# Performance work log

Measured on AMD Instinct MI355X. Metric: run time of the kernel, lower is better.

## Reference

```python
import jax, jax.numpy as jnp
import numpy as np

C = 1024
T = 2048
B = 8

def setup_inputs() -> dict:
    key = jax.random.key(0)
    ks = jax.random.split(key, 7)
    s = lambda fan_in: 1.0 / np.sqrt(fan_in)
    return {
        "x":     jax.random.normal(ks[0], (B, T, C), dtype=jnp.float32),
        "w_qkv": jax.random.uniform(ks[1], (C, 3 * C), jnp.float32, -s(C), s(C)),
        "w_proj": jax.random.uniform(ks[2], (C, C), jnp.float32, -s(C), s(C)),
        "w1":    jax.random.uniform(ks[3], (C, 2 * C), jnp.float32, -s(C), s(C)),
        "w2":    jax.random.uniform(ks[4], (2 * C, C), jnp.float32, -s(2 * C), s(2 * C)),
        "g1":    jnp.ones((C,), jnp.float32),
        "g2":    jnp.ones((C,), jnp.float32),
    }

def rmsnorm(x, g, eps=1e-6):
    return x * jax.lax.rsqrt(jnp.mean(x * x, axis=-1, keepdims=True) + eps) * g

def reference(x, w_qkv, w_proj, w1, w2, g1, g2):
    t = x.shape[1]
    # --- attention ---
    h = rmsnorm(x, g1)
    qkv = h @ w_qkv                               # [B,T,3C]
    q, k, v = jnp.split(qkv, 3, axis=-1)
    scores = jnp.einsum('bqc,bkc->bqk', q, k) * (C ** -0.5)  # [B,T,T]
    causal = jnp.triu(jnp.ones((t, t), dtype=bool), k=1)
    scores = jnp.where(causal, -jnp.inf, scores)
    attn = jax.nn.softmax(scores, axis=-1)
    x = x + (attn @ v) @ w_proj
    # --- ffn ---
    h = rmsnorm(x, g2)
    return x + (jax.nn.silu(h @ w1)) @ w2
```

## Files before the change

kernel.cpp:

```cpp
#include <hip/hip_runtime.h>
#include <hip/hip_bf16.h>
#include <stdint.h>


#define C_DIM 1024
#define T_DIM 2048
#define B_DIM 8

typedef float f32x4  __attribute__((ext_vector_type(4)));
typedef float f32x16 __attribute__((ext_vector_type(16)));
typedef __bf16 bf16x8 __attribute__((ext_vector_type(8)));

typedef const __attribute__((address_space(1))) void gvoid_t;
typedef __attribute__((address_space(3))) void lvoid_t;

__device__ __forceinline__ void gload_lds16(const void* g, void* l) {
    __builtin_amdgcn_global_load_lds((gvoid_t*)g, (lvoid_t*)l, 16, 0, 0);
}

__device__ __forceinline__ unsigned short f2bf_bits(float f) {
    __hip_bfloat16 h = __float2bfloat16(f);
    return *reinterpret_cast<unsigned short*>(&h);
}

__device__ __forceinline__ void xcd_remap(int& bx, int& by, int& bz) {
    const int gx = gridDim.x, gy = gridDim.y;
    const int nwg = gx * gy * (int)gridDim.z;
    const int orig = bx + gx * (by + gy * bz);
    const int q = nwg >> 3, r = nwg & 7;
    const int xcd = orig & 7, pos = orig >> 3;
    const int neu = (xcd < r ? xcd * (q + 1) : r * (q + 1) + (xcd - r) * q) + pos;
    bx = neu % gx;
    const int t = neu / gx;
    by = t % gy;
    bz = t / gy;
}

#define RD_A(dst, buf, hq) do { \
    _Pragma("unroll") \
    for (int mf_ = 0; mf_ < 4; ++mf_) { \
        const char* p_ = lds + (buf)*32768 + wrb + (hq)*8192 + mf_*2048; \
        dst[mf_][0] = *(const bf16x8*)(p_ + offk0); \
        dst[mf_][1] = *(const bf16x8*)(p_ + offk1); \
    } \
} while(0)

#define RD_B(dst, buf, nh) do { \
    _Pragma("unroll") \
    for (int n2_ = 0; n2_ < 2; ++n2_) { \
        const char* p_ = lds + 65536 + (buf)*32768 + wcb + ((nh)*2 + n2_)*2048; \
        dst[n2_][0] = *(const bf16x8*)(p_ + offk0); \
        dst[n2_][1] = *(const bf16x8*)(p_ + offk1); \
    } \
} while(0)

#define MMQ(aS, bS, Mh, Nh) do { \
    _Pragma("unroll") \
    for (int m4_ = 0; m4_ < 4; ++m4_) \
    _Pragma("unroll") \
    for (int n2_ = 0; n2_ < 2; ++n2_) \
    _Pragma("unroll") \
    for (int ks_ = 0; ks_ < 2; ++ks_) \
        acc[(Mh)*4 + m4_][(Nh)*2 + n2_] = __builtin_amdgcn_mfma_f32_16x16x32_bf16( \
            aS[m4_][ks_], bS[n2_][ks_], acc[(Mh)*4 + m4_][(Nh)*2 + n2_], 0, 0, 0); \
} while(0)

#define STA(buf, half, kt) do { \
    const int go_ = aoff + (half)*128*lda + (kt)*64; \
    char* lp_ = ldsw + (buf)*32768 + (half)*16384; \
    gload_lds16(A + go_,            lp_); \
    gload_lds16(A + go_ + 64*lda,   lp_ + 8192); \
} while(0)
#define STB(buf, half, kt) do { \
    const int go_ = boff + (half)*128*ldb + (kt)*64; \
    char* lp_ = ldsw + 65536 + (buf)*32768 + (half)*16384; \
    gload_lds16(Bt + go_,           lp_); \
    gload_lds16(Bt + go_ + 64*ldb,  lp_ + 8192); \
} while(0)

#define TILE_BODY(t, STG) do { \
    const int buf_ = (t) & 1; \
    bf16x8 a0[4][2], a1[4][2], b0v[2][2], b1v[2][2]; \
    RD_A(a0, buf_, 0); RD_A(a1, buf_, 1); \
    RD_B(b0v, buf_, 0); RD_B(b1v, buf_, 1); \
    __builtin_amdgcn_s_setprio(1); \
    MMQ(a0, b0v, 0, 0); MMQ(a0, b1v, 0, 1); \
    MMQ(a1, b0v, 1, 0); MMQ(a1, b1v, 1, 1); \
    __builtin_amdgcn_s_setprio(0); \
    asm volatile("s_waitcnt lgkmcnt(0)" ::: "memory"); \
    asm volatile("s_waitcnt vmcnt(0)" ::: "memory"); \
    __builtin_amdgcn_s_barrier(); \
    if (STG) { STB(buf_,0,(t)+2); STB(buf_,1,(t)+2); \
               STA(buf_,0,(t)+2); STA(buf_,1,(t)+2); } \
} while(0)

template<int EPI>
__global__ __launch_bounds__(512, 2)
void gemm256(const __hip_bfloat16* A, const __hip_bfloat16* Bt,
             void* Cout, const void* Rv,
             int K, int lda, int ldb, int ldc)
{
    int bx = blockIdx.x, by = blockIdx.y, bz = blockIdx.z;
    xcd_remap(bx, by, bz);

    const int tid  = threadIdx.x;
    const int lane = tid & 63, wave = tid >> 6;
    const int l15  = lane & 15, l4 = lane >> 4;
    const int wr   = wave >> 2, wc = wave & 3;
    const int m0   = by * 256, n0 = bx * 256;

    __shared__ __align__(16) char lds_[131072];
    char* lds  = lds_;
    char* ldsw = lds_ + wave * 1024;

    const int NT = K >> 6;

    const int offk0 = l15 * 128 + (((l4)     ^ (l15 & 7)) << 4);
    const int offk1 = l15 * 128 + (((4 + l4) ^ (l15 & 7)) << 4);
    const int wrb = wr * 16384, wcb = wc * 8192;

    const int rowq  = tid >> 3;
    const int sslot = (tid & 7) ^ (rowq & 7);
    const int aoff  = (m0 + rowq) * lda + sslot * 8;
    const int boff  = (n0 + rowq) * ldb + sslot * 8;

    f32x4 acc[8][4];
#pragma unroll
    for (int i = 0; i < 8; ++i)
#pragma unroll
        for (int j = 0; j < 4; ++j) acc[i][j] = (f32x4){0.f, 0.f, 0.f, 0.f};

    STB(0, 0, 0); STB(0, 1, 0); STA(0, 0, 0); STA(0, 1, 0);
    STB(1, 0, 1); STB(1, 1, 1); STA(1, 0, 1); STA(1, 1, 1);
    asm volatile("s_waitcnt vmcnt(8)" ::: "memory");
    __builtin_amdgcn_s_barrier();

    int t = 0;
    for (; t < NT - 2; ++t) TILE_BODY(t, true);
    for (; t < NT; ++t)     TILE_BODY(t, false);

    asm volatile("s_waitcnt vmcnt(0)" ::: "memory");

#pragma unroll
    for (int mf = 0; mf < 8; ++mf) {
        const int rbase = m0 + wr * 128 + mf * 16 + l4 * 4;
#pragma unroll
        for (int nf = 0; nf < 4; ++nf) {
            const int col = n0 + wc * 64 + nf * 16 + l15;
#pragma unroll
            for (int r = 0; r < 4; ++r) {
                const float v = acc[mf][nf][r];
                const int row = rbase + r;
                if constexpr (EPI == 5) {
                    ((__hip_bfloat16*)Cout)[((long long)(row >> 11) * C_DIM + col) * T_DIM
                                            + (row & 2047)] = __float2bfloat16(v);
                } else {
                    const long long idx = (long long)row * ldc + col;
                    if constexpr (EPI == 0) {
                        ((__hip_bfloat16*)Cout)[idx] = __float2bfloat16(v);
                    } else if constexpr (EPI == 3) {
                        const float s = v / (1.f + __expf(-v));
                        ((__hip_bfloat16*)Cout)[idx] = __float2bfloat16(s);
                    } else if constexpr (EPI == 8) {
                        const float xr = ((const float*)Rv)[idx];
                        ((__hip_bfloat16*)Cout)[idx] = __float2bfloat16(v + xr);
                    } else {
                        const float xr =
                            __bfloat162float(((const __hip_bfloat16*)Rv)[idx]);
                        ((float*)Cout)[idx] = v + xr;
                    }
                }
            }
        }
    }
}

__global__ __launch_bounds__(512, 2)
void gemm256_w32(const __hip_bfloat16* A, const __hip_bfloat16* Bt,
                 void* Cout, int K, int lda, int ldb, int ldc)
{
    int bx = blockIdx.x, by = blockIdx.y, bz = blockIdx.z;
    xcd_remap(bx, by, bz);

    const int tid  = threadIdx.x;
    const int lane = tid & 63, wave = tid >> 6;
    const int l31  = lane & 31, l5 = lane >> 5;
    const int wr   = wave >> 2, wc = wave & 3;
    const int m0   = by * 256, n0 = bx * 256;

    __shared__ __align__(16) char lds_[131072];
    char* lds  = lds_;
    char* ldsw = lds_ + wave * 1024;

    const int NT = K >> 6;

    const int rowq  = tid >> 3;
    const int sslot = (tid & 7) ^ (rowq & 7);
    const int aoff  = (m0 + rowq) * lda + sslot * 8;
    const int boff  = (n0 + rowq) * ldb + sslot * 8;

    f32x16 acc[4][2];
#pragma unroll
    for (int i = 0; i < 4; ++i)
#pragma unroll
        for (int j = 0; j < 2; ++j)
#pragma unroll
            for (int e = 0; e < 16; ++e) acc[i][j][e] = 0.f;

    const int arowl = l31 & 7;

    STB(0, 0, 0); STB(0, 1, 0); STA(0, 0, 0); STA(0, 1, 0);
    STB(1, 0, 1); STB(1, 1, 1); STA(1, 0, 1); STA(1, 1, 1);
    asm volatile("s_waitcnt vmcnt(8)" ::: "memory");
    __builtin_amdgcn_s_barrier();

    for (int t = 0; t < NT; ++t) {
        const int buf_ = t & 1;
        bf16x8 aR[4][4], bR[2][4];
#pragma unroll
        for (int mf = 0; mf < 4; ++mf) {
            const int arow = wr * 128 + mf * 32 + l31;
            const char* p_ = lds + buf_ * 32768 + arow * 128;
#pragma unroll
            for (int ks = 0; ks < 4; ++ks)
                aR[mf][ks] = *(const bf16x8*)(p_ + ((((ks << 1) | l5) ^ arowl) << 4));
        }
#pragma unroll
        for (int nf = 0; nf < 2; ++nf) {
            const int bcol = wc * 64 + nf * 32 + l31;
            const char* p_ = lds + 65536 + buf_ * 32768 + bcol * 128;
#pragma unroll
            for (int ks = 0; ks < 4; ++ks)
                bR[nf][ks] = *(const bf16x8*)(p_ + ((((ks << 1) | l5) ^ arowl) << 4));
        }
        __builtin_amdgcn_s_setprio(1);
#pragma unroll
        for (int mf = 0; mf < 4; ++mf)
#pragma unroll
            for (int nf = 0; nf < 2; ++nf)
#pragma unroll
                for (int ks = 0; ks < 4; ++ks)
                    acc[mf][nf] = __builtin_amdgcn_mfma_f32_32x32x16_bf16(
                        aR[mf][ks], bR[nf][ks], acc[mf][nf], 0, 0, 0);
        __builtin_amdgcn_s_setprio(0);
        asm volatile("s_waitcnt lgkmcnt(0)" ::: "memory");
        asm volatile("s_waitcnt vmcnt(0)" ::: "memory");
        __builtin_amdgcn_s_barrier();
        if (t + 2 < NT) {
            STB(buf_, 0, t + 2); STB(buf_, 1, t + 2);
            STA(buf_, 0, t + 2); STA(buf_, 1, t + 2);
        }
    }
    asm volatile("s_waitcnt vmcnt(0)" ::: "memory");

#pragma unroll
    for (int mf = 0; mf < 4; ++mf)
#pragma unroll
        for (int nf = 0; nf < 2; ++nf) {
            const int col = n0 + wc * 64 + nf * 32 + l31;
#pragma unroll
            for (int reg = 0; reg < 16; ++reg) {
                const int row = m0 + wr * 128 + mf * 32
                              + (reg & 3) + 8 * (reg >> 2) + 4 * l5;
                ((__hip_bfloat16*)Cout)[(long long)row * ldc + col] =
                    __float2bfloat16(acc[mf][nf][reg]);
            }
        }
}

template<int EPI, int CMODE>
__global__ __launch_bounds__(256)
void gemm128(const __hip_bfloat16* A, const __hip_bfloat16* Bt,
             void* Cout, int K, int lda, int ldb, int ldc,
             long long sA, long long sB, long long sC, float scale)
{
    int bx = blockIdx.x, by = blockIdx.y, bz = blockIdx.z;
    xcd_remap(bx, by, bz);
    if constexpr (CMODE == 1) { if (bx > by) return; }

    const int tid  = threadIdx.x;
    const int lane = tid & 63, wave = tid >> 6;
    const int l15  = lane & 15, l4 = lane >> 4;
    const int wr   = wave >> 1, wc = wave & 1;
    const int m0   = by * 128, n0 = bx * 128;
    const int z    = bz;

    A  += (long long)z * sA;
    Bt += (long long)z * sB;

    __shared__ __align__(16) short As[2][128 * 32];
    __shared__ __align__(16) short Bs[2][128 * 32];

    int kmax = K;
    if constexpr (CMODE == 2) { int km = m0 + 128; kmax = km < K ? km : K; }

    f32x4 acc[4][4];
#pragma unroll
    for (int i = 0; i < 4; ++i)
#pragma unroll
        for (int j = 0; j < 4; ++j) acc[i][j] = (f32x4){0.f, 0.f, 0.f, 0.f};

    const int srow  = wave * 32 + (lane >> 2);
    const int sbyte = (((lane & 3) ^ ((lane >> 2) & 3))) << 4;
    const char* Ag = (const char*)(A  + (long long)(m0 + srow) * lda) + sbyte;
    const char* Bg = (const char*)(Bt + (long long)(n0 + srow) * ldb) + sbyte;
    const long long astep = (long long)16 * lda * 2;
    const long long bstep = (long long)16 * ldb * 2;
    char* AsW[2] = {(char*)As[0] + wave * 2048, (char*)As[1] + wave * 2048};
    char* BsW[2] = {(char*)Bs[0] + wave * 2048, (char*)Bs[1] + wave * 2048};

    auto stage = [&](int buf, int k0) {
        const char* ag = Ag + (long long)k0 * 2;
        const char* bg = Bg + (long long)k0 * 2;
        gload_lds16(ag,         AsW[buf]);
        gload_lds16(ag + astep, AsW[buf] + 1024);
        gload_lds16(bg,         BsW[buf]);
        gload_lds16(bg + bstep, BsW[buf] + 1024);
    };

    const int cs16 = ((l4 ^ (l15 & 3)) << 4);

    stage(0, 0);
    __syncthreads();

    for (int k0 = 0; k0 < kmax; k0 += 32) {
        const int buf = (k0 >> 5) & 1;
        if (k0 + 32 < kmax) stage(buf ^ 1, k0 + 32);

        const char* Ac = (const char*)As[buf];
        const char* Bc = (const char*)Bs[buf];
        bf16x8 af[4], bfr[4];
#pragma unroll
        for (int mi = 0; mi < 4; ++mi) {
            int row = wr * 64 + mi * 16 + l15;
            af[mi] = *(const bf16x8*)(Ac + row * 64 + cs16);
        }
#pragma unroll
        for (int ni = 0; ni < 4; ++ni) {
            int col = wc * 64 + ni * 16 + l15;
            bfr[ni] = *(const bf16x8*)(Bc + col * 64 + cs16);
        }
#pragma unroll
        for (int mi = 0; mi < 4; ++mi)
#pragma unroll
            for (int ni = 0; ni < 4; ++ni)
                acc[mi][ni] = __builtin_amdgcn_mfma_f32_16x16x32_bf16(
                    af[mi], bfr[ni], acc[mi][ni], 0, 0, 0);

        __syncthreads();
    }

    const long long cbase = (long long)z * sC;
#pragma unroll
    for (int mi = 0; mi < 4; ++mi) {
        const int rbase = m0 + wr * 64 + mi * 16 + l4 * 4;
#pragma unroll
        for (int ni = 0; ni < 4; ++ni) {
            const int col = n0 + wc * 64 + ni * 16 + l15;
#pragma unroll
            for (int r = 0; r < 4; ++r) {
                const long long idx = cbase + (long long)(rbase + r) * ldc + col;
                const float v = acc[mi][ni][r];
                if constexpr (EPI == 0) {
                    ((__hip_bfloat16*)Cout)[idx] = __float2bfloat16(v);
                } else {
                    ((__hip_bfloat16*)Cout)[idx] = __float2bfloat16(v * scale);
                }
            }
        }
    }
}

template<bool BF16IN>
__global__ __launch_bounds__(256)
void rmsnorm_kernel(const void* __restrict__ xin, const float* __restrict__ g,
                    __hip_bfloat16* __restrict__ out)
{
    const long long row = blockIdx.x;
    const int tid = threadIdx.x;
    float e0, e1, e2, e3;
    if constexpr (BF16IN) {
        const ushort4 u = ((const ushort4*)((const __hip_bfloat16*)xin + row * C_DIM))[tid];
        e0 = __uint_as_float((unsigned)u.x << 16);
        e1 = __uint_as_float((unsigned)u.y << 16);
        e2 = __uint_as_float((unsigned)u.z << 16);
        e3 = __uint_as_float((unsigned)u.w << 16);
    } else {
        const float4 v = ((const float4*)((const float*)xin + row * C_DIM))[tid];
        e0 = v.x; e1 = v.y; e2 = v.z; e3 = v.w;
    }
    float ss = e0 * e0 + e1 * e1 + e2 * e2 + e3 * e3;
#pragma unroll
    for (int off = 32; off; off >>= 1) ss += __shfl_xor(ss, off);
    __shared__ float red[4];
    if ((tid & 63) == 0) red[tid >> 6] = ss;
    __syncthreads();
    ss = red[0] + red[1] + red[2] + red[3];
    const float sc = rsqrtf(ss * (1.0f / C_DIM) + 1e-6f);
    const float4 gv = ((const float4*)g)[tid];
    ushort4 u;
    u.x = f2bf_bits(e0 * sc * gv.x);
    u.y = f2bf_bits(e1 * sc * gv.y);
    u.z = f2bf_bits(e2 * sc * gv.z);
    u.w = f2bf_bits(e3 * sc * gv.w);
    *(ushort4*)(out + row * C_DIM + tid * 4) = u;
}

__global__ __launch_bounds__(256)
void softmax_causal(__hip_bfloat16* __restrict__ SP)
{
    const int i = blockIdx.x, b = blockIdx.y;
    __hip_bfloat16* row = SP + ((long long)b * T_DIM + i) * T_DIM;
    const int tid = threadIdx.x;
    const int jbase = tid * 8;
    const int kmax = ((i >> 7) + 1) << 7;
    const bool act = jbase < kmax;

    float v[8];
    if (act) {
        uint4 raw = ((const uint4*)row)[tid];
        const unsigned w[4] = {raw.x, raw.y, raw.z, raw.w};
#pragma unroll
        for (int c = 0; c < 4; ++c) {
            v[2 * c]     = __uint_as_float(w[c] << 16);
            v[2 * c + 1] = __uint_as_float(w[c] & 0xFFFF0000u);
        }
#pragma unroll
        for (int e = 0; e < 8; ++e)
            if (jbase + e > i) v[e] = -1e30f;
    } else {
#pragma unroll
        for (int e = 0; e < 8; ++e) v[e] = -1e30f;
    }

    float m = v[0];
#pragma unroll
    for (int e = 1; e < 8; ++e) m = fmaxf(m, v[e]);
#pragma unroll
    for (int off = 32; off; off >>= 1) m = fmaxf(m, __shfl_xor(m, off));
    __shared__ float redm[4], reds[4];
    if ((tid & 63) == 0) redm[tid >> 6] = m;
    __syncthreads();
    m = fmaxf(fmaxf(redm[0], redm[1]), fmaxf(redm[2], redm[3]));

    float e8[8];
    float s = 0.f;
#pragma unroll
    for (int e = 0; e < 8; ++e) { e8[e] = __expf(v[e] - m); s += e8[e]; }
#pragma unroll
    for (int off = 32; off; off >>= 1) s += __shfl_xor(s, off);
    if ((tid & 63) == 0) reds[tid >> 6] = s;
    __syncthreads();
    s = reds[0] + reds[1] + reds[2] + reds[3];
    const float inv = 1.f / s;

    if (act) {
        uint4 outw;
        unsigned o[4];
#pragma unroll
        for (int c = 0; c < 4; ++c) {
            unsigned lo = f2bf_bits(e8[2 * c] * inv);
            unsigned hi = f2bf_bits(e8[2 * c + 1] * inv);
            o[c] = lo | (hi << 16);
        }
        outw.x = o[0]; outw.y = o[1]; outw.z = o[2]; outw.w = o[3];
        ((uint4*)row)[tid] = outw;
    }
}

__global__ __launch_bounds__(256)
void wcast_t(const float* __restrict__ in, __hip_bfloat16* __restrict__ out,
             int K, int N)
{
    __shared__ float t[32][33];
    const int n0 = blockIdx.x * 32, k0 = blockIdx.y * 32;
    const int tx = threadIdx.x, ty = threadIdx.y;
#pragma unroll
    for (int r = ty; r < 32; r += 8)
        t[r][tx] = in[(long long)(k0 + r) * N + n0 + tx];
    __syncthreads();
#pragma unroll
    for (int r = ty; r < 32; r += 8)
        out[(long long)(n0 + r) * K + k0 + tx] = __float2bfloat16(t[tx][r]);
}

extern "C" void kernel_launch(void* const* d_in, const int* in_sizes, int n_in,
                              void* d_out, int out_size, void* d_ws, size_t ws_size,
                              hipStream_t stream)
{
    const float* x      = (const float*)d_in[0];
    const float* w_qkv  = (const float*)d_in[1];
    const float* w_proj = (const float*)d_in[2];
    const float* w1     = (const float*)d_in[3];
    const float* w2     = (const float*)d_in[4];
    const float* g1     = (const float*)d_in[5];
    const float* g2     = (const float*)d_in[6];
    float* out = (float*)d_out;
    char* ws = (char*)d_ws;

    const size_t SP_off = 0;
    const size_t h_off  = 0;
    const size_t u_off  = 0;
    const size_t q_off  = 67108864ull;
    const size_t k_off  = 100663296ull;
    const size_t vT_off = 134217728ull;
    const size_t wq_off = 167772160ull;
    const size_t wp_off = wq_off + 6291456ull;
    const size_t w1_off = wp_off + 2097152ull;
    const size_t w2_off = w1_off + 4194304ull;
    const size_t NEED   = w2_off + 4194304ull;

    if (ws_size < NEED) return;

    auto bf = [&](size_t off) { return (__hip_bfloat16*)(ws + off); };

    wcast_t<<<dim3(96, 32), dim3(32, 8), 0, stream>>>(w_qkv,  bf(wq_off), 1024, 3072);
    wcast_t<<<dim3(32, 32), dim3(32, 8), 0, stream>>>(w_proj, bf(wp_off), 1024, 1024);
    wcast_t<<<dim3(64, 32), dim3(32, 8), 0, stream>>>(w1,     bf(w1_off), 1024, 2048);
    wcast_t<<<dim3(32, 64), dim3(32, 8), 0, stream>>>(w2,     bf(w2_off), 2048, 1024);

    rmsnorm_kernel<false><<<16384, 256, 0, stream>>>(x, g1, bf(h_off));

    gemm256_w32<<<dim3(4, 64, 1), 512, 0, stream>>>(
        bf(h_off), bf(wq_off), bf(q_off), 1024, 1024, 1024, 1024);
    gemm256<0><<<dim3(4, 64, 1), 512, 0, stream>>>(
        bf(h_off), bf(wq_off) + 1024 * 1024, bf(k_off), nullptr,
        1024, 1024, 1024, 1024);
    gemm256<5><<<dim3(4, 64, 1), 512, 0, stream>>>(
        bf(h_off), bf(wq_off) + 2 * 1024 * 1024, bf(vT_off), nullptr,
        1024, 1024, 1024, 2048);

    gemm128<4, 1><<<dim3(16, 16, 8), 256, 0, stream>>>(
        bf(q_off), bf(k_off), bf(SP_off),
        1024, 1024, 1024, 2048,
        (long long)T_DIM * C_DIM, (long long)T_DIM * C_DIM, (long long)T_DIM * T_DIM,
        0.03125f);

    softmax_causal<<<dim3(2048, 8), 256, 0, stream>>>(bf(SP_off));

    gemm128<0, 2><<<dim3(8, 16, 8), 256, 0, stream>>>(
        bf(SP_off), bf(vT_off), bf(k_off) ,
        2048, 2048, 2048, 1024,
        (long long)T_DIM * T_DIM, (long long)C_DIM * T_DIM, (long long)T_DIM * C_DIM,
        1.f);

    gemm256<8><<<dim3(4, 64, 1), 512, 0, stream>>>(
        bf(k_off) , bf(wp_off), bf(vT_off) , x,
        1024, 1024, 1024, 1024);

    rmsnorm_kernel<true><<<16384, 256, 0, stream>>>(bf(vT_off), g2, bf(q_off));

    gemm256<3><<<dim3(8, 64, 1), 512, 0, stream>>>(
        bf(q_off), bf(w1_off), bf(u_off), nullptr,
        1024, 1024, 1024, 2048);

    gemm256<9><<<dim3(4, 64, 1), 512, 0, stream>>>(
        bf(u_off), bf(w2_off), out, bf(vT_off) ,
        2048, 2048, 2048, 1024);
}
```

Baseline: 499.2 us.

## Split GEMM main loop into eight-phase ping-pong schedule with staggered loads

Restructures the 256x256 bf16 GEMM inner loop into four quadrant phases separated by barriers. Each phase issues part of the next tile's global-to-LDS loads and the next LDS register read, then runs one MFMA quadrant. This replaces the single full vmcnt(0) wait per tile with partial waits, and it prefetches the A fragment for the next tile. The aim is to overlap memory traffic with matrix math, at the cost of many more barriers and extra fragment registers live at once.

```diff
diff --git a/kernel.cpp b/kernel.cpp
--- a/kernel.cpp
+++ b/kernel.cpp
@@ -78,27 +78,43 @@
     gload_lds16(Bt + go_ + 64*ldb,  lp_ + 8192); \
 } while(0)
 
-#define TILE_BODY(t, STG) do { \
+#define BAR_RAW() __builtin_amdgcn_s_barrier()
+#define LGKM0_RAW() asm volatile("s_waitcnt lgkmcnt(0)" ::: "memory")
+
+#define TILE8(t, STG) do { \
     const int buf_ = (t) & 1; \
-    bf16x8 a0[4][2], a1[4][2], b0v[2][2], b1v[2][2]; \
-    RD_A(a0, buf_, 0); RD_A(a1, buf_, 1); \
-    RD_B(b0v, buf_, 0); RD_B(b1v, buf_, 1); \
-    __builtin_amdgcn_s_setprio(1); \
-    MMQ(a0, b0v, 0, 0); MMQ(a0, b1v, 0, 1); \
-    MMQ(a1, b0v, 1, 0); MMQ(a1, b1v, 1, 1); \
-    __builtin_amdgcn_s_setprio(0); \
-    asm volatile("s_waitcnt lgkmcnt(0)" ::: "memory"); \
-    asm volatile("s_waitcnt vmcnt(0)" ::: "memory"); \
-    __builtin_amdgcn_s_barrier(); \
-    if (STG) { STB(buf_,0,(t)+2); STB(buf_,1,(t)+2); \
-               STA(buf_,0,(t)+2); STA(buf_,1,(t)+2); } \
+     \
+    RD_B(bL, buf_, 0); \
+    BAR_RAW(); LGKM0_RAW(); \
+    __builtin_amdgcn_s_setprio(1); MMQ(aX, bL, 0, 0); __builtin_amdgcn_s_setprio(0); \
+    BAR_RAW(); \
+     \
+    if (STG) STB(buf_, 0, (t) + 2); \
+    RD_B(bH, buf_, 1); \
+    BAR_RAW(); LGKM0_RAW(); \
+    __builtin_amdgcn_s_setprio(1); MMQ(aX, bH, 0, 1); __builtin_amdgcn_s_setprio(0); \
+    BAR_RAW(); \
+     \
+    if (STG) STB(buf_, 1, (t) + 2); \
+    RD_A(aY, buf_, 1); \
+    BAR_RAW(); LGKM0_RAW(); \
+    __builtin_amdgcn_s_setprio(1); MMQ(aY, bH, 1, 1); __builtin_amdgcn_s_setprio(0); \
+    if (STG) { asm volatile("s_waitcnt vmcnt(4)" ::: "memory"); } \
+    else     { asm volatile("s_waitcnt vmcnt(0)" ::: "memory"); } \
+    BAR_RAW(); \
+     \
+    if (STG) { STA(buf_, 0, (t) + 2); STA(buf_, 1, (t) + 2); } \
+    if ((t) + 1 < NT) RD_A(aX, buf_ ^ 1, 0); \
+    BAR_RAW(); LGKM0_RAW(); \
+    __builtin_amdgcn_s_setprio(1); MMQ(aY, bL, 1, 0); __builtin_amdgcn_s_setprio(0); \
+    BAR_RAW(); \
 } while(0)
 
 template<int EPI>
 __global__ __launch_bounds__(512, 2)
-void gemm256(const __hip_bfloat16* A, const __hip_bfloat16* Bt,
-             void* Cout, const void* Rv,
-             int K, int lda, int ldb, int ldc)
+void gemm256_8p(const __hip_bfloat16* A, const __hip_bfloat16* Bt,
+                void* Cout, const void* Rv,
+                int K, int lda, int ldb, int ldc)
 {
     int bx = blockIdx.x, by = blockIdx.y, bz = blockIdx.z;
     xcd_remap(bx, by, bz);
@@ -129,15 +145,17 @@
     for (int i = 0; i < 8; ++i)
 #pragma unroll
         for (int j = 0; j < 4; ++j) acc[i][j] = (f32x4){0.f, 0.f, 0.f, 0.f};
+    bf16x8 aX[4][2], aY[4][2], bL[2][2], bH[2][2];
 
     STB(0, 0, 0); STB(0, 1, 0); STA(0, 0, 0); STA(0, 1, 0);
     STB(1, 0, 1); STB(1, 1, 1); STA(1, 0, 1); STA(1, 1, 1);
     asm volatile("s_waitcnt vmcnt(8)" ::: "memory");
-    __builtin_amdgcn_s_barrier();
+    BAR_RAW();
+    RD_A(aX, 0, 0);
 
     int t = 0;
-    for (; t < NT - 2; ++t) TILE_BODY(t, true);
-    for (; t < NT; ++t)     TILE_BODY(t, false);
+    for (; t < NT - 2; ++t) TILE8(t, true);
+    for (; t < NT; ++t)     TILE8(t, false);
 
     asm volatile("s_waitcnt vmcnt(0)" ::: "memory");
 
@@ -523,10 +541,10 @@
 
     gemm256_w32<<<dim3(4, 64, 1), 512, 0, stream>>>(
         bf(h_off), bf(wq_off), bf(q_off), 1024, 1024, 1024, 1024);
-    gemm256<0><<<dim3(4, 64, 1), 512, 0, stream>>>(
+    gemm256_8p<0><<<dim3(4, 64, 1), 512, 0, stream>>>(
         bf(h_off), bf(wq_off) + 1024 * 1024, bf(k_off), nullptr,
         1024, 1024, 1024, 1024);
-    gemm256<5><<<dim3(4, 64, 1), 512, 0, stream>>>(
+    gemm256_8p<5><<<dim3(4, 64, 1), 512, 0, stream>>>(
         bf(h_off), bf(wq_off) + 2 * 1024 * 1024, bf(vT_off), nullptr,
         1024, 1024, 1024, 2048);
 
@@ -544,17 +562,17 @@
         (long long)T_DIM * T_DIM, (long long)C_DIM * T_DIM, (long long)T_DIM * C_DIM,
         1.f);
 
-    gemm256<8><<<dim3(4, 64, 1), 512, 0, stream>>>(
+    gemm256_8p<8><<<dim3(4, 64, 1), 512, 0, stream>>>(
         bf(k_off) , bf(wp_off), bf(vT_off) , x,
         1024, 1024, 1024, 1024);
 
     rmsnorm_kernel<true><<<16384, 256, 0, stream>>>(bf(vT_off), g2, bf(q_off));
 
-    gemm256<3><<<dim3(8, 64, 1), 512, 0, stream>>>(
+    gemm256_8p<3><<<dim3(8, 64, 1), 512, 0, stream>>>(
         bf(q_off), bf(w1_off), bf(u_off), nullptr,
         1024, 1024, 1024, 2048);
 
-    gemm256<9><<<dim3(4, 64, 1), 512, 0, stream>>>(
+    gemm256_8p<9><<<dim3(4, 64, 1), 512, 0, stream>>>(
         bf(u_off), bf(w2_off), out, bf(vT_off) ,
         2048, 2048, 2048, 1024);
 }
```

Result: no change. 503.2 us (+0.8%).
